# Kernel optimization log

Hardware: AMD Instinct MI355X
Metric: run time of the kernel (lower is better)

Reference implementation:

```python
import jax, jax.numpy as jnp
import numpy as np

# Hyperparameters matching init_kwargs
DIM = 1024
HEADS = 16
MEM_HIDDEN = 512
FF_DIM = 4096
CHUNK = 128
NPERSIST = 16
ALPHA = 0.02
THETA = 0.1
ETA = 0.9
B, T = 2, 1024


def _mem_read(x, p):
    """DeepMemory forward: 2-layer MLP dim->hidden->dim with SiLU between."""
    W1, b1, W2, b2 = p
    h = jax.nn.silu(x @ W1.T + b1)
    return h @ W2.T + b2


def setup_inputs() -> dict:
    key = jax.random.key(0)
    ks = jax.random.split(key, 16)
    s = 0.02  # weight init scale
    return {
        "x": jax.random.normal(ks[0], (B, T, DIM), jnp.float32),
        "Wqkv": jax.random.normal(ks[1], (3 * DIM, DIM), jnp.float32) * s,
        "mW1": jax.random.normal(ks[2], (MEM_HIDDEN, DIM), jnp.float32) * s,
        "mb1": jnp.zeros((MEM_HIDDEN,), jnp.float32),
        "mW2": jax.random.normal(ks[3], (DIM, MEM_HIDDEN), jnp.float32) * s,
        "mb2": jnp.zeros((DIM,), jnp.float32),
        "P": jax.random.normal(ks[4], (1, NPERSIST, DIM), jnp.float32),
        "Wqkv_attn": jax.random.normal(ks[5], (3 * DIM, DIM), jnp.float32) * s,
        "Wo": jax.random.normal(ks[6], (DIM, DIM), jnp.float32) * s,
        "ffW1": jax.random.normal(ks[7], (FF_DIM, DIM), jnp.float32) * s,
        "ffb1": jnp.zeros((FF_DIM,), jnp.float32),
        "ffW2": jax.random.normal(ks[8], (DIM, FF_DIM), jnp.float32) * s,
        "ffb2": jnp.zeros((DIM,), jnp.float32),
    }


def reference(x, Wqkv, mW1, mb1, mW2, mb2, P, Wqkv_attn, Wo, ffW1, ffb1, ffW2, ffb2):
    Bb, Tt, D = x.shape
    nC = Tt // CHUNK

    # shared qkv projection (bias-free Linear)
    qkv = x @ Wqkv.T                       # [B,T,3D]
    K = qkv[..., D:2 * D]
    V = qkv[..., 2 * D:]

    # chunked test-time memory writes: k,v are detached in the torch code
    Kc = jax.lax.stop_gradient(K).reshape(Bb, nC, CHUNK, D).transpose(1, 0, 2, 3)  # [nC,B,C,D]
    Vc = jax.lax.stop_gradient(V).reshape(Bb, nC, CHUNK, D).transpose(1, 0, 2, 3)

    params0 = tuple(jax.lax.stop_gradient(p) for p in (mW1, mb1, mW2, mb2))
    mom0 = tuple(jnp.zeros_like(p) for p in params0)

    def loss_fn(p, k, v):
        return jnp.mean((_mem_read(k, p) - v) ** 2)

    def step(carry, kv):
        p, m = carry
        k, v = kv
        g = jax.grad(loss_fn)(p, k, v)
        # momentum: s = eta*s - theta*g ; weight: w = (1-alpha)*w + s
        m = tuple(ETA * mi - THETA * gi for mi, gi in zip(m, g))
        p = tuple((1.0 - ALPHA) * pi + mi for pi, mi in zip(p, m))
        return (p, m), None

    (pf, _), _ = jax.lax.scan(step, (params0, mom0), (Kc, Vc))
    pf = jax.lax.stop_gradient(pf)  # fast weights are buffers (non-differentiable)

    # memory readout tokens for the whole segment
    Q = qkv[..., :D]
    mem_tok = _mem_read(Q, pf)             # [B,T,D]

    # concatenate persistent + memory + input tokens
    tokens = jnp.concatenate([jnp.broadcast_to(P, (Bb, NPERSIST, D)), mem_tok, x], axis=1)
    N = tokens.shape[1]                    # NPERSIST + 2T
    dh = D // HEADS

    # causal multi-head attention over the concatenated sequence
    aqkv = tokens @ Wqkv_attn.T            # [B,N,3D]
    q, k, v = jnp.split(aqkv, 3, axis=-1)
    to_heads = lambda t: t.reshape(Bb, N, HEADS, dh).transpose(0, 2, 1, 3)
    q, k, v = to_heads(q), to_heads(k), to_heads(v)
    scores = jnp.einsum('bhnd,bhmd->bhnm', q, k) / jnp.sqrt(jnp.float32(dh))
    causal = jnp.tril(jnp.ones((N, N), bool))
    scores = jnp.where(causal, scores, jnp.float32(-1e9))
    attn = jax.nn.softmax(scores, axis=-1)
    o = jnp.einsum('bhnm,bhmd->bhnd', attn, v).transpose(0, 2, 1, 3).reshape(Bb, N, D)
    y = o @ Wo.T

    # feed-forward (no residual in source)
    y = jax.nn.gelu(y @ ffW1.T + ffb1) @ ffW2.T + ffb2

    # drop persistent + memory tokens, gate by a fresh memory read
    out = y[:, NPERSIST + Tt:, :]          # [B,T,D]
    newQ = (out @ Wqkv.T)[..., :D]
    return out * _mem_read(newQ, pf)
```

## Files before the change

### kernel.cpp

```cpp
#include <hip/hip_runtime.h>
#include <math.h>

#define BATCH 2
#define TSEQ 1024
#define DIMD 1024
#define NPERS 16
#define NCH 8
#define NTOK 2064
#define ETA_C 0.9f
#define THETA_C 0.1f
#define ALPHA_C 0.02f

typedef __attribute__((ext_vector_type(4))) float f32x4;
typedef __attribute__((ext_vector_type(8))) short s16x8;
typedef unsigned short u16;

__device__ __forceinline__ u16 f2bf(float f) {
    unsigned int u = __float_as_uint(f);
    return (u16)((u + 0x7fffu + ((u >> 16) & 1u)) >> 16);
}
__device__ __forceinline__ float bf2f(u16 h) { return __uint_as_float(((unsigned)h) << 16); }
__device__ __forceinline__ void split2(float v, u16& h, u16& l) {
    h = f2bf(v); l = f2bf(v - bf2f(h));
}

static const size_t oRA = 0;
static const size_t oRB = 50724864;
static const size_t oRC = 67633152;
static const size_t oRD = 80216064;
static const size_t oRE = 96993280;
static const size_t oRF = 109576192;
static const size_t oRG = 113770496;
static const size_t oRH = 117970944;

static const size_t PW1 = 0, PB1 = 524288, PW2 = 524800, PB2 = 1049088, PSZ = 1050112;

__device__ __forceinline__ void gload_lds16(const u16* g, u16* l) {
    __builtin_amdgcn_global_load_lds(
        (const __attribute__((address_space(1))) unsigned int*)g,
        (__attribute__((address_space(3))) unsigned int*)l, 16, 0, 0);
}

__device__ __forceinline__ void xcd_swizzle(int& bx, int& by) {
    int gx = gridDim.x, nwg = gx * gridDim.y;
    int lid = blockIdx.y * gx + blockIdx.x;
    int t = lid;
    if ((nwg & 7) == 0) {
        int q = nwg >> 3;
        t = (lid & 7) * q + (lid >> 3);
    }
    bx = t % gx; by = t / gx;
}

__device__ __forceinline__ void stage_tile(const u16* sp, u16* buf, int rbase,
                                           int M, int clampM, int K, int k0,
                                           int wid, int lane) {
    const int lr = lane >> 2, lc = lane & 3;
    #pragma unroll
    for (int i = 0; i < 8; ++i) {
        int r = i * 16 + lr;
        int gr = rbase + r;
        if (clampM && gr >= M) gr = M - 1;
        int g = lc ^ ((r >> 1) & 3);
        gload_lds16(sp + (size_t)gr * K + k0 + g * 8, buf + wid * 4096 + i * 512);
    }
}

__device__ __forceinline__ void stage_tile64(const u16* sp, u16* buf, int rbase,
                                             int K, int k0, int wid, int lane) {
    const int lr = lane >> 3, lc = lane & 7;
    #pragma unroll
    for (int i = 0; i < 16; ++i) {
        int r = i * 8 + lr;
        int gr = rbase + r;
        int g = lc ^ (r & 7);
        gload_lds16(sp + (size_t)gr * K + k0 + g * 8, buf + wid * 8192 + i * 512);
    }
}

template<int NPROD>
__device__ __forceinline__ void mm_loop32(u16 lds[2][16384],
                const u16* sp, int rbase, int M, int clampM, int K,
                int kbeg, int kend, int wid, int lane, int wm, int wn,
                f32x4 acc[4][4]) {
    const int frow = lane & 15, kblk = lane >> 4;
    const int nt = (kend - kbeg) >> 5;
    const int doStage = (NPROD == 3) || (wid != 1);
    if (doStage) stage_tile(sp, lds[0], rbase, M, clampM, K, kbeg, wid, lane);
    for (int t = 0; t < nt; ++t) {
        __syncthreads();
        if (t + 1 < nt && doStage)
            stage_tile(sp, lds[(t + 1) & 1], rbase, M, clampM, K, kbeg + ((t + 1) << 5), wid, lane);
        const u16* cb = lds[t & 1];
        s16x8 bh[4], bl[4];
        #pragma unroll
        for (int ni = 0; ni < 4; ++ni) {
            int br = wn * 64 + ni * 16 + frow;
            int pc = kblk ^ ((br >> 1) & 3);
            bh[ni] = *(const s16x8*)&cb[2 * 4096 + br * 32 + pc * 8];
            bl[ni] = *(const s16x8*)&cb[3 * 4096 + br * 32 + pc * 8];
        }
        #pragma unroll
        for (int mi = 0; mi < 4; ++mi) {
            int ar = wm * 64 + mi * 16 + frow;
            int pc = kblk ^ ((ar >> 1) & 3);
            s16x8 ah = *(const s16x8*)&cb[0 * 4096 + ar * 32 + pc * 8];
            s16x8 al;
            if (NPROD == 3) al = *(const s16x8*)&cb[1 * 4096 + ar * 32 + pc * 8];
            #pragma unroll
            for (int ni = 0; ni < 4; ++ni) {
                acc[mi][ni] = __builtin_amdgcn_mfma_f32_16x16x32_bf16(ah, bh[ni], acc[mi][ni], 0, 0, 0);
                acc[mi][ni] = __builtin_amdgcn_mfma_f32_16x16x32_bf16(ah, bl[ni], acc[mi][ni], 0, 0, 0);
                if (NPROD == 3)
                    acc[mi][ni] = __builtin_amdgcn_mfma_f32_16x16x32_bf16(al, bh[ni], acc[mi][ni], 0, 0, 0);
            }
        }
    }
}

template<int ACTF, int WF32, int WSPLIT, int PARTIAL, int NPROD>
__global__ __launch_bounds__(256)
void gemm_mfma_k(const u16* __restrict__ Ah, const u16* __restrict__ Al,
                 const u16* __restrict__ Wh, const u16* __restrict__ Wl,
                 float* __restrict__ C, u16* __restrict__ Chi, u16* __restrict__ Clo,
                 int M, int N, int K, const float* __restrict__ bias)
{
    __shared__ u16 lds[2][16384];
    const int tid = threadIdx.x;
    const int lane = tid & 63, wid = tid >> 6;
    const int wm = wid >> 1, wn = wid & 1;
    int bx, by; xcd_swizzle(bx, by);
    const int row0 = by * 128, col0 = bx * 128;
    const u16* sp = (wid == 0) ? Ah : (wid == 1) ? Al : (wid == 2) ? Wh : Wl;
    const int rbase = (wid < 2) ? row0 : col0;
    const int clampM = (wid < 2) ? 1 : 0;
    f32x4 acc[4][4] = {};
    int kbeg = 0, kend = K;
    if (PARTIAL) {
        int Kseg = K / gridDim.z;
        kbeg = blockIdx.z * Kseg;
        kend = kbeg + Kseg;
    }
    mm_loop32<NPROD>(lds, sp, rbase, M, clampM, K, kbeg, kend, wid, lane, wm, wn, acc);

    const int erow = (lane >> 4) * 4, ecol = lane & 15;
    #pragma unroll
    for (int mi = 0; mi < 4; ++mi) {
        #pragma unroll
        for (int ni = 0; ni < 4; ++ni) {
            int c = col0 + wn * 64 + ni * 16 + ecol;
            float bv = (!PARTIAL && bias) ? bias[c] : 0.f;
            #pragma unroll
            for (int reg = 0; reg < 4; ++reg) {
                int r = row0 + wm * 64 + mi * 16 + erow + reg;
                if (r >= M) continue;
                float v = acc[mi][ni][reg] + bv;
                if (PARTIAL) {
                    C[((size_t)blockIdx.z * M + r) * N + c] = v;
                    continue;
                }
                if (ACTF == 1) v = v / (1.f + __expf(-v));
                else if (ACTF == 2) {
                    float u = 0.7978845608028654f * (v + 0.044715f * v * v * v);
                    v = 0.5f * v * (1.f + tanhf(u));
                }
                size_t o = (size_t)r * N + c;
                if (WF32) C[o] = v;
                if (WSPLIT) { u16 h, l; split2(v, h, l); Chi[o] = h; Clo[o] = l; }
            }
        }
    }
}

__global__ __launch_bounds__(256)
void gemm_qkv_k(const u16* __restrict__ Ah, const u16* __restrict__ Al,
                const u16* __restrict__ Wh, const u16* __restrict__ Wl,
                u16* __restrict__ Qh, u16* __restrict__ Ql,
                u16* __restrict__ kch, u16* __restrict__ kcl,
                u16* __restrict__ kcTh, u16* __restrict__ kcTl,
                float* __restrict__ Vb, int M, int N, int K)
{
    __shared__ u16 lds[2][16384];
    const int tid = threadIdx.x;
    const int lane = tid & 63, wid = tid >> 6;
    const int wm = wid >> 1, wn = wid & 1;
    int bx, by; xcd_swizzle(bx, by);
    const int row0 = by * 128, col0 = bx * 128;
    const u16* sp = (wid == 0) ? Ah : (wid == 1) ? Al : (wid == 2) ? Wh : Wl;
    const int rbase = (wid < 2) ? row0 : col0;
    f32x4 acc[4][4] = {};
    mm_loop32<3>(lds, sp, rbase, M, 0, K, 0, K, wid, lane, wm, wn, acc);

    const int erow = (lane >> 4) * 4, ecol = lane & 15;
    #pragma unroll
    for (int mi = 0; mi < 4; ++mi) {
        #pragma unroll
        for (int ni = 0; ni < 4; ++ni) {
            int c = col0 + wn * 64 + ni * 16 + ecol;
            #pragma unroll
            for (int reg = 0; reg < 4; ++reg) {
                int r = row0 + wm * 64 + mi * 16 + erow + reg;
                float v = acc[mi][ni][reg];
                int b = r >> 10, t = r & 1023;
                if (c < 1024) {
                    size_t o = (size_t)r * 1024 + c;
                    u16 h, l; split2(v, h, l); Qh[o] = h; Ql[o] = l;
                } else if (c < 2048) {
                    int d = c - 1024;
                    int ch = t >> 7, rr = t & 127;
                    size_t o = ((size_t)((ch * 2 + b) * 128 + rr)) * 1024 + d;
                    u16 h, l; split2(v, h, l);
                    kch[o] = h; kcl[o] = l;
                    size_t ot = (size_t)ch * 262144 + (size_t)d * 256 + b * 128 + rr;
                    kcTh[ot] = h; kcTl[ot] = l;
                } else {
                    int d = c - 2048;
                    int ch = t >> 7, rr = t & 127;
                    Vb[((size_t)((ch * 2 + b) * 128 + rr)) * 1024 + d] = v;
                }
            }
        }
    }
}

__global__ __launch_bounds__(256)
void gemm_aqkv_k(const u16* __restrict__ Ah, const u16* __restrict__ Al,
                 const u16* __restrict__ Wh, const u16* __restrict__ Wl,
                 u16* __restrict__ fQh, u16* __restrict__ fQl,
                 u16* __restrict__ fKh, u16* __restrict__ fKl,
                 u16* __restrict__ fVt, int M, int N, int K)
{
    __shared__ u16 lds[2][16384];
    const int tid = threadIdx.x;
    const int lane = tid & 63, wid = tid >> 6;
    const int wm = wid >> 1, wn = wid & 1;
    int bx, by; xcd_swizzle(bx, by);
    if (bx < 8 && ((by <= 7) || (by >= 17 && by <= 23))) return;
    const int row0 = by * 128, col0 = bx * 128;
    const u16* sp = (wid == 0) ? Ah : (wid == 1) ? Al : (wid == 2) ? Wh : Wl;
    const int rbase = (wid < 2) ? row0 : col0;
    const int clampM = (wid < 2) ? 1 : 0;
    f32x4 acc[4][4] = {};
    mm_loop32<2>(lds, sp, rbase, M, clampM, K, 0, K, wid, lane, wm, wn, acc);

    const int erow = (lane >> 4) * 4, ecol = lane & 15;
    #pragma unroll
    for (int mi = 0; mi < 4; ++mi) {
        #pragma unroll
        for (int ni = 0; ni < 4; ++ni) {
            int c = col0 + wn * 64 + ni * 16 + ecol;
            #pragma unroll
            for (int reg = 0; reg < 4; ++reg) {
                int r = row0 + wm * 64 + mi * 16 + erow + reg;
                if (r >= M) continue;
                float v = acc[mi][ni][reg];
                int b = (r >= 2064) ? 1 : 0;
                int n = r - b * 2064;
                if (c < 1024) {
                    if (n >= NPERS + TSEQ) {
                        int h = c >> 6, d = c & 63;
                        int row = n - (NPERS + TSEQ);
                        size_t o = (((size_t)(b * 16 + h)) * 1024 + row) * 64 + d;
                        u16 hh, ll; split2(0.125f * v, hh, ll);
                        fQh[o] = hh; fQl[o] = ll;
                    }
                } else if (c < 2048) {
                    int cc = c - 1024;
                    int h = cc >> 6, d = cc & 63;
                    size_t o = (((size_t)(b * 16 + h)) * NTOK + n) * 64 + d;
                    u16 hh, ll; split2(v, hh, ll);
                    fKh[o] = hh; fKl[o] = ll;
                } else {
                    int cc = c - 2048;
                    int h = cc >> 6, d = cc & 63;
                    fVt[(((size_t)(b * 16 + h)) * 64 + d) * NTOK + n] = f2bf(v);
                }
            }
        }
    }
}

template<int ACTF, int WF32, int WSPLIT>
__global__ __launch_bounds__(256)
void reduce_k(const float* __restrict__ Cp, int S,
              float* __restrict__ C, u16* __restrict__ Chi, u16* __restrict__ Clo,
              const float* __restrict__ bias, int M, int N)
{
    int i = blockIdx.x * 256 + threadIdx.x;
    int n4 = (int)((size_t)M * N / 4);
    if (i >= n4) return;
    size_t off = (size_t)i * 4;
    float4 v = *(const float4*)&Cp[off];
    for (int z = 1; z < S; ++z) {
        float4 u = *(const float4*)&Cp[(size_t)z * M * N + off];
        v.x += u.x; v.y += u.y; v.z += u.z; v.w += u.w;
    }
    int c = (int)(off % N);
    float vv[4] = {v.x, v.y, v.z, v.w};
    #pragma unroll
    for (int j = 0; j < 4; ++j) {
        float w = vv[j];
        if (bias) w += bias[c + j];
        if (ACTF == 1) w = w / (1.f + __expf(-w));
        else if (ACTF == 2) {
            float u = 0.7978845608028654f * (w + 0.044715f * w * w * w);
            w = 0.5f * w * (1.f + tanhf(u));
        }
        if (WF32) C[off + j] = w;
        if (WSPLIT) { u16 h, l; split2(w, h, l); Chi[off + j] = h; Clo[off + j] = l; }
    }
}

static void gemm_mfma(hipStream_t s, int act, int wf32, int wsplit,
                      const u16* Ah, const u16* Al, const u16* Wh, const u16* Wl,
                      float* C, u16* Ch, u16* Cl, int M, int N, int K,
                      const float* bias, int nprod = 3)
{
    dim3 g(N / 128, (M + 127) / 128), b(256);
    if (act == 0 && wf32 == 1 && wsplit == 0)
        gemm_mfma_k<0,1,0,0,3><<<g,b,0,s>>>(Ah,Al,Wh,Wl,C,Ch,Cl,M,N,K,bias);
    else if (act == 0 && wf32 == 1 && wsplit == 1)
        gemm_mfma_k<0,1,1,0,3><<<g,b,0,s>>>(Ah,Al,Wh,Wl,C,Ch,Cl,M,N,K,bias);
    else if (act == 0 && wf32 == 0 && wsplit == 1)
        gemm_mfma_k<0,0,1,0,3><<<g,b,0,s>>>(Ah,Al,Wh,Wl,C,Ch,Cl,M,N,K,bias);
    else if (act == 1)
        gemm_mfma_k<1,0,1,0,3><<<g,b,0,s>>>(Ah,Al,Wh,Wl,C,Ch,Cl,M,N,K,bias);
    else if (nprod == 2)
        gemm_mfma_k<2,0,1,0,2><<<g,b,0,s>>>(Ah,Al,Wh,Wl,C,Ch,Cl,M,N,K,bias);
    else
        gemm_mfma_k<2,0,1,0,3><<<g,b,0,s>>>(Ah,Al,Wh,Wl,C,Ch,Cl,M,N,K,bias);
}

static void gemm_mfma_sk(hipStream_t s, int act, int wf32, int wsplit,
                         const u16* Ah, const u16* Al, const u16* Wh, const u16* Wl,
                         float* C, u16* Ch, u16* Cl, int M, int N, int K,
                         const float* bias, int S, float* part, int nprod = 3)
{
    if (S <= 1) { gemm_mfma(s, act, wf32, wsplit, Ah, Al, Wh, Wl, C, Ch, Cl, M, N, K, bias, nprod); return; }
    dim3 g(N / 128, (M + 127) / 128, S), b(256);
    if (nprod == 2)
        gemm_mfma_k<0,0,0,1,2><<<g,b,0,s>>>(Ah,Al,Wh,Wl,part,nullptr,nullptr,M,N,K,nullptr);
    else
        gemm_mfma_k<0,0,0,1,3><<<g,b,0,s>>>(Ah,Al,Wh,Wl,part,nullptr,nullptr,M,N,K,nullptr);
    int n4 = (int)((size_t)M * N / 4);
    dim3 rg((n4 + 255) / 256), rb(256);
    if (act == 0 && wf32 == 1 && wsplit == 0)
        reduce_k<0,1,0><<<rg,rb,0,s>>>(part, S, C, Ch, Cl, bias, M, N);
    else if (act == 0 && wf32 == 1 && wsplit == 1)
        reduce_k<0,1,1><<<rg,rb,0,s>>>(part, S, C, Ch, Cl, bias, M, N);
    else if (act == 0 && wf32 == 0 && wsplit == 1)
        reduce_k<0,0,1><<<rg,rb,0,s>>>(part, S, C, Ch, Cl, bias, M, N);
    else if (act == 1)
        reduce_k<1,0,1><<<rg,rb,0,s>>>(part, S, C, Ch, Cl, bias, M, N);
    else
        reduce_k<2,0,1><<<rg,rb,0,s>>>(part, S, C, Ch, Cl, bias, M, N);
}

template<int MODE>
__device__ __forceinline__ void scan_body(u16* lds, int bx, int by,
                 const u16* __restrict__ Ah, const u16* __restrict__ Al,
                 const u16* __restrict__ Wh, const u16* __restrict__ Wl,
                 float* __restrict__ C, u16* __restrict__ Chi, u16* __restrict__ Clo,
                 u16* __restrict__ ChiT, u16* __restrict__ CloT,
                 const float* __restrict__ Zf, const float* __restrict__ add,
                 const float* __restrict__ bias, float* __restrict__ CP,
                 int M, int N, int K, float alpha)
{
    const int tid = threadIdx.x;
    const int lane = tid & 63, wid = tid >> 6;
    const int wm = wid >> 1, wn = wid & 1;
    const int row0 = by * 128, col0 = bx * 128;

    const u16* sp = (wid == 0) ? Ah : (wid == 1) ? Al : (wid == 2) ? Wh : Wl;
    const int rbase = (wid < 2) ? row0 : col0;

    f32x4 acc[4][4] = {};
    const int frow = lane & 15, kblk = lane >> 4;
    const int nt = K >> 6;

    stage_tile64(sp, lds, rbase, K, 0, wid, lane);

    for (int t = 0; t < nt; ++t) {
        __syncthreads();
        if (t + 1 < nt)
            stage_tile64(sp, lds + (((t + 1) & 1) << 15), rbase, K, (t + 1) << 6, wid, lane);
        const u16* cb = lds + ((t & 1) << 15);

        #pragma unroll
        for (int s = 0; s < 2; ++s) {
            s16x8 bh[4], bl[4];
            #pragma unroll
            for (int ni = 0; ni < 4; ++ni) {
                int br = wn * 64 + ni * 16 + frow;
                int pc = (s * 4 + kblk) ^ (br & 7);
                bh[ni] = *(const s16x8*)&cb[2 * 8192 + br * 64 + pc * 8];
                bl[ni] = *(const s16x8*)&cb[3 * 8192 + br * 64 + pc * 8];
            }
            #pragma unroll
            for (int mi = 0; mi < 4; ++mi) {
                int ar = wm * 64 + mi * 16 + frow;
                int pc = (s * 4 + kblk) ^ (ar & 7);
                s16x8 ah = *(const s16x8*)&cb[0 * 8192 + ar * 64 + pc * 8];
                s16x8 al = *(const s16x8*)&cb[1 * 8192 + ar * 64 + pc * 8];
                #pragma unroll
                for (int ni = 0; ni < 4; ++ni) {
                    acc[mi][ni] = __builtin_amdgcn_mfma_f32_16x16x32_bf16(ah, bh[ni], acc[mi][ni], 0, 0, 0);
                    acc[mi][ni] = __builtin_amdgcn_mfma_f32_16x16x32_bf16(ah, bl[ni], acc[mi][ni], 0, 0, 0);
                    acc[mi][ni] = __builtin_amdgcn_mfma_f32_16x16x32_bf16(al, bh[ni], acc[mi][ni], 0, 0, 0);
                }
            }
        }
    }

    const int erow = (lane >> 4) * 4, ecol = lane & 15;
    float csum[4] = {0.f, 0.f, 0.f, 0.f};
    #pragma unroll
    for (int mi = 0; mi < 4; ++mi) {
        #pragma unroll
        for (int ni = 0; ni < 4; ++ni) {
            int c = col0 + wn * 64 + ni * 16 + ecol;
            #pragma unroll
            for (int reg = 0; reg < 4; ++reg) {
                int r = row0 + wm * 64 + mi * 16 + erow + reg;
                float v = acc[mi][ni][reg];
                size_t o = (size_t)r * N + c;
                if (MODE == 1) {
                    v += bias[c];
                    C[o] = v;
                    float hv = v / (1.f + __expf(-v));
                    u16 h, l; split2(hv, h, l);
                    Chi[o] = h; Clo[o] = l;
                    size_t ot = (size_t)c * M + r;
                    ChiT[ot] = h; CloT[ot] = l;
                } else if (MODE == 2) {
                    v += bias[c] - add[o];
                    u16 h, l; split2(v, h, l);
                    Chi[o] = h; Clo[o] = l;
                    size_t ot = (size_t)c * M + r;
                    ChiT[ot] = h; CloT[ot] = l;
                    csum[ni] += v;
                } else if (MODE == 3) {
                    C[o] = alpha * v;
                } else {
                    v *= alpha;
                    float z = Zf[o];
                    float sg = 1.f / (1.f + __expf(-z));
                    v *= sg * (1.f + z * (1.f - sg));
                    u16 h, l; split2(v, h, l);
                    size_t ot = (size_t)c * M + r;
                    ChiT[ot] = h; CloT[ot] = l;
                    csum[ni] += v;
                }
            }
        }
    }
    if (MODE == 2 || MODE == 4) {
        #pragma unroll
        for (int ni = 0; ni < 4; ++ni) {
            float s = csum[ni];
            s += __shfl_xor(s, 16);
            s += __shfl_xor(s, 32);
            if ((lane >> 4) == 0) {
                int c = col0 + wn * 64 + ni * 16 + ecol;
                float w = (MODE == 2) ? alpha * s : s;
                CP[(size_t)(by * 2 + wm) * N + c] = w;
            }
        }
    }
}

template<int MODE>
__global__ __launch_bounds__(256)
void gemm_scan_k(const u16* __restrict__ Ah, const u16* __restrict__ Al,
                 const u16* __restrict__ Wh, const u16* __restrict__ Wl,
                 float* __restrict__ C, u16* __restrict__ Chi, u16* __restrict__ Clo,
                 u16* __restrict__ ChiT, u16* __restrict__ CloT,
                 const float* __restrict__ Zf, const float* __restrict__ add,
                 const float* __restrict__ bias, float* __restrict__ CP,
                 int M, int N, int K, float alpha)
{
    __shared__ u16 lds[2][32768];
    int bx, by; xcd_swizzle(bx, by);
    scan_body<MODE>(&lds[0][0], bx, by, Ah, Al, Wh, Wl, C, Chi, Clo, ChiT, CloT,
                    Zf, add, bias, CP, M, N, K, alpha);
}

__global__ __launch_bounds__(256)
void gemm_scan_pair_k(const u16* __restrict__ rTh, const u16* __restrict__ rTl,
                      const u16* __restrict__ hTh, const u16* __restrict__ hTl,
                      float* __restrict__ gW2,
                      const u16* __restrict__ rh_, const u16* __restrict__ rl_,
                      const u16* __restrict__ w2th, const u16* __restrict__ w2tl,
                      u16* __restrict__ dhTh, u16* __restrict__ dhTl,
                      const float* __restrict__ z1, float* __restrict__ cp1, float cs)
{
    __shared__ u16 lds[2][32768];
    if (blockIdx.y < 8) {
        scan_body<3>(&lds[0][0], blockIdx.x, blockIdx.y, rTh, rTl, hTh, hTl,
                     gW2, nullptr, nullptr, nullptr, nullptr, nullptr, nullptr,
                     nullptr, nullptr, 1024, 512, 256, cs);
    } else {
        scan_body<4>(&lds[0][0], blockIdx.x, blockIdx.y - 8, rh_, rl_, w2th, w2tl,
                     nullptr, nullptr, nullptr, dhTh, dhTl, z1, nullptr,
                     nullptr, cp1, 256, 512, 1024, cs);
    }
}

__global__ void cvt_split_k(const float* __restrict__ in, u16* __restrict__ hi,
                            u16* __restrict__ lo, int n4) {
    int i = blockIdx.x * 256 + threadIdx.x;
    if (i >= n4) return;
    float4 v = *(const float4*)&in[(size_t)i * 4];
    u16 h0,l0,h1,l1,h2,l2,h3,l3;
    split2(v.x,h0,l0); split2(v.y,h1,l1); split2(v.z,h2,l2); split2(v.w,h3,l3);
    ushort4 hv = {h0,h1,h2,h3}, lv = {l0,l1,l2,l3};
    *(ushort4*)&hi[(size_t)i * 4] = hv;
    *(ushort4*)&lo[(size_t)i * 4] = lv;
}
__global__ void transpose_split_k(const float* __restrict__ in, u16* __restrict__ outh,
                                  u16* __restrict__ outl, int R, int C) {
    __shared__ float t[32][33];
    const int c0 = blockIdx.x * 32, r0 = blockIdx.y * 32;
    const size_t zoff = (size_t)blockIdx.z * R * C;
    const int tx = threadIdx.x & 31, ty = threadIdx.x >> 5;
    #pragma unroll
    for (int p = 0; p < 4; ++p) {
        int r = ty + p * 8;
        t[r][tx] = in[zoff + (size_t)(r0 + r) * C + c0 + tx];
    }
    __syncthreads();
    #pragma unroll
    for (int p = 0; p < 4; ++p) {
        int cc = ty + p * 8;
        float v = t[tx][cc];
        u16 h, l; split2(v, h, l);
        size_t o = zoff + (size_t)(c0 + cc) * R + r0 + tx;
        outh[o] = h; outl[o] = l;
    }
}
__global__ void update3_k(float* __restrict__ p, float* __restrict__ mo,
                          const float* __restrict__ g,
                          const float* __restrict__ cp1, const float* __restrict__ cp2,
                          u16* __restrict__ w1h, u16* __restrict__ w1l,
                          u16* __restrict__ w2h, u16* __restrict__ w2l,
                          u16* __restrict__ w2th, u16* __restrict__ w2tl, int n) {
    int i = blockIdx.x * 256 + threadIdx.x;
    if (i >= n) return;
    float gi;
    if (i < 524288) gi = g[i];
    else if (i < 524800) {
        int j = i - 524288;
        gi = cp1[j] + cp1[512 + j] + cp1[1024 + j] + cp1[1536 + j];
    } else if (i < 1049088) gi = g[i];
    else {
        int j = i - 1049088;
        gi = cp2[j] + cp2[1024 + j] + cp2[2048 + j] + cp2[3072 + j];
    }
    float m = ETA_C * mo[i] - THETA_C * gi;
    mo[i] = m;
    float pv = (1.f - ALPHA_C) * p[i] + m;
    p[i] = pv;
    if (i < 524288) {
        u16 h, l; split2(pv, h, l); w1h[i] = h; w1l[i] = l;
    } else if (i >= 524800 && i < 1049088) {
        int j = i - 524800;
        u16 h, l; split2(pv, h, l);
        w2h[j] = h; w2l[j] = l;
        int tj = (j & 511) * 1024 + (j >> 9);
        w2th[tj] = h; w2tl[tj] = l;
    }
}
__global__ void tokens_split_k(const float* __restrict__ P, const float* __restrict__ memtok,
                               const float* __restrict__ x, u16* __restrict__ th,
                               u16* __restrict__ tl) {
    size_t idx = (size_t)blockIdx.x * 256 + threadIdx.x;
    int d = (int)(idx & 1023);
    int n = (int)((idx >> 10) % NTOK);
    int b = (int)(idx / ((size_t)NTOK * 1024));
    float v;
    if (n < NPERS)            v = P[(size_t)n * 1024 + d];
    else if (n < NPERS + TSEQ) v = memtok[((size_t)b * TSEQ + (n - NPERS)) * 1024 + d];
    else                      v = x[((size_t)b * TSEQ + (n - NPERS - TSEQ)) * 1024 + d];
    u16 h, l; split2(v, h, l); th[idx] = h; tl[idx] = l;
}
__global__ void mul_k(const float* __restrict__ a, const float* __restrict__ b,
                      float* __restrict__ o, int n) {
    int i = blockIdx.x * 256 + threadIdx.x;
    if (i < n) o[i] = a[i] * b[i];
}

__global__ __launch_bounds__(256)
void flash_part_k(const u16* __restrict__ Qsh, const u16* __restrict__ Qsl,
                  const u16* __restrict__ Ksh, const u16* __restrict__ Ksl,
                  const u16* __restrict__ Vts, float* __restrict__ Of,
                  float* __restrict__ Mf, float* __restrict__ Lf)
{
    __shared__ u16 lds[20480];
    u16* KH = lds;            u16* KL = lds + 4096;
    u16* VT = lds + 8192;
    u16* PH = lds + 12288;    u16* PL = lds + 16384;

    int lid = blockIdx.x + (blockIdx.y << 4) + (blockIdx.z << 8);
    int t1024 = ((lid & 7) << 7) | (lid >> 3);
    const int qt = t1024 & 15, h = (t1024 >> 4) & 15;
    const int zb = t1024 >> 8;
    const int b = zb >> 1, z = zb & 1;

    const int tid = threadIdx.x;
    const int lane = tid & 63, wid = tid >> 6;
    const int fr = lane & 15, kq = lane >> 4;
    const int bh = b * 16 + h;
    const int q0c = qt * 64;
    const int q0a = NPERS + TSEQ + q0c;
    const int ntile = ((q0a + 63) >> 6) + 1;
    const int half = ntile >> 1;
    const int jt0 = z ? half : 0;
    const int jt1 = z ? ntile : half;
    const int l8 = lane & 7, lr8 = lane >> 3;

    auto stageKV = [&](int jt) {
        const int j0 = jt * 64;
        #pragma unroll
        for (int jj = 0; jj < 6; ++jj) {
            int j = wid * 6 + jj;
            int buf = j >> 3, i8 = j & 7;
            if (buf < 2) {
                int row = i8 * 8 + lr8;
                int grow = j0 + row; if (grow > NTOK - 1) grow = NTOK - 1;
                int c = l8 ^ (row & 7);
                const u16* src = (buf == 0 ? Ksh : Ksl) +
                                 (((size_t)bh * NTOK + grow) << 6) + c * 8;
                gload_lds16(src, (buf == 0 ? KH : KL) + i8 * 512);
            } else {
                int d = i8 * 8 + lr8;
                int c = l8 ^ (d & 7);
                int col = j0 + c * 8; if (col > NTOK - 8) col = NTOK - 8;
                const u16* src = Vts + ((size_t)bh * 64 + d) * NTOK + col;
                gload_lds16(src, VT + i8 * 512);
            }
        }
    };

    s16x8 qh[2], ql[2];
    {
        const size_t qrow = ((size_t)bh * 1024 + q0c + wid * 16 + fr) << 6;
        #pragma unroll
        for (int kb = 0; kb < 2; ++kb) {
            qh[kb] = *(const s16x8*)&Qsh[qrow + (size_t)(kb * 4 + kq) * 8];
            ql[kb] = *(const s16x8*)&Qsl[qrow + (size_t)(kb * 4 + kq) * 8];
        }
    }

    f32x4 Oa[4] = {};
    float mrow[4], lrow[4];
    #pragma unroll
    for (int r = 0; r < 4; ++r) { mrow[r] = -INFINITY; lrow[r] = 0.f; }

    for (int jt = jt0; jt < jt1; ++jt) {
        const int j0 = jt * 64;
        stageKV(jt);
        __syncthreads();

        f32x4 sacc[4] = {};
        __builtin_amdgcn_s_setprio(1);
        #pragma unroll
        for (int nt = 0; nt < 4; ++nt) {
            #pragma unroll
            for (int kb = 0; kb < 2; ++kb) {
                int br = nt * 16 + fr;
                int sl = (kb * 4 + kq) ^ (fr & 7);
                s16x8 kh = *(const s16x8*)&KH[br * 64 + sl * 8];
                s16x8 kl = *(const s16x8*)&KL[br * 64 + sl * 8];
                sacc[nt] = __builtin_amdgcn_mfma_f32_16x16x32_bf16(qh[kb], kh, sacc[nt], 0, 0, 0);
                sacc[nt] = __builtin_amdgcn_mfma_f32_16x16x32_bf16(ql[kb], kh, sacc[nt], 0, 0, 0);
                sacc[nt] = __builtin_amdgcn_mfma_f32_16x16x32_bf16(qh[kb], kl, sacc[nt], 0, 0, 0);
            }
        }
        __builtin_amdgcn_s_setprio(0);

        #pragma unroll
        for (int r = 0; r < 4; ++r) {
            const int qloc = kq * 4 + r;
            const int qi = q0a + wid * 16 + qloc;
            float sv[4], tmax = -INFINITY;
            #pragma unroll
            for (int nt = 0; nt < 4; ++nt) {
                int kj = j0 + nt * 16 + fr;
                sv[nt] = (kj <= qi) ? sacc[nt][r] : -INFINITY;
                tmax = fmaxf(tmax, sv[nt]);
            }
            #pragma unroll
            for (int off = 1; off < 16; off <<= 1)
                tmax = fmaxf(tmax, __shfl_xor(tmax, off));
            float mnew = fmaxf(mrow[r], tmax);
            float scale = __expf(mrow[r] - mnew);
            float psum = 0.f;
            float p4[4];
            #pragma unroll
            for (int nt = 0; nt < 4; ++nt) { p4[nt] = __expf(sv[nt] - mnew); psum += p4[nt]; }
            #pragma unroll
            for (int off = 1; off < 16; off <<= 1)
                psum += __shfl_xor(psum, off);
            lrow[r] = lrow[r] * scale + psum;
            mrow[r] = mnew;
            #pragma unroll
            for (int dt = 0; dt < 4; ++dt) Oa[dt][r] *= scale;
            const int prow = wid * 16 + qloc;
            #pragma unroll
            for (int nt = 0; nt < 4; ++nt) {
                u16 ph, pl; split2(p4[nt], ph, pl);
                int col = nt * 16 + fr;
                int sl = (col >> 3) ^ (qloc & 7);
                int off = prow * 64 + sl * 8 + (col & 7);
                PH[off] = ph; PL[off] = pl;
            }
        }

        __builtin_amdgcn_s_setprio(1);
        #pragma unroll
        for (int kb = 0; kb < 2; ++kb) {
            int pr = wid * 16 + fr;
            int sl = (kb * 4 + kq) ^ (fr & 7);
            s16x8 pa = *(const s16x8*)&PH[pr * 64 + sl * 8];
            s16x8 pb = *(const s16x8*)&PL[pr * 64 + sl * 8];
            #pragma unroll
            for (int dt = 0; dt < 4; ++dt) {
                int vr = dt * 16 + fr;
                s16x8 vb = *(const s16x8*)&VT[vr * 64 + sl * 8];
                Oa[dt] = __builtin_amdgcn_mfma_f32_16x16x32_bf16(pa, vb, Oa[dt], 0, 0, 0);
                Oa[dt] = __builtin_amdgcn_mfma_f32_16x16x32_bf16(pb, vb, Oa[dt], 0, 0, 0);
            }
        }
        __builtin_amdgcn_s_setprio(0);
        __syncthreads();
    }

    const size_t obase = ((((size_t)z * 2 + b) * 16 + h) * 16 + qt) * 4096;
    const size_t mlb   = ((((size_t)z * 2 + b) * 16 + h) * 16 + qt) * 64;
    #pragma unroll
    for (int r = 0; r < 4; ++r) {
        int rl = wid * 16 + kq * 4 + r;
        if (fr == 0) { Mf[mlb + rl] = mrow[r]; Lf[mlb + rl] = lrow[r]; }
        #pragma unroll
        for (int dt = 0; dt < 4; ++dt)
            Of[obase + (size_t)rl * 64 + dt * 16 + fr] = Oa[dt][r];
    }
}

__global__ __launch_bounds__(256)
void flash_merge_k(const float* __restrict__ Of, const float* __restrict__ Mf,
                   const float* __restrict__ Lf, u16* __restrict__ oh, u16* __restrict__ ol)
{
    const int qt = blockIdx.x, h = blockIdx.y, b = blockIdx.z;
    const int tid = threadIdx.x;
    const int row = tid >> 2, quad = tid & 3;
    const size_t b0 = ((((size_t)0 * 2 + b) * 16 + h) * 16 + qt) * 4096 + (size_t)row * 64;
    const size_t b1 = ((((size_t)1 * 2 + b) * 16 + h) * 16 + qt) * 4096 + (size_t)row * 64;
    const size_t m0i = ((((size_t)0 * 2 + b) * 16 + h) * 16 + qt) * 64 + row;
    const size_t m1i = ((((size_t)1 * 2 + b) * 16 + h) * 16 + qt) * 64 + row;
    float m0 = Mf[m0i], m1 = Mf[m1i], l0 = Lf[m0i], l1 = Lf[m1i];
    float m = fmaxf(m0, m1);
    float e0 = __expf(m0 - m), e1 = __expf(m1 - m);
    float inv = 1.f / (l0 * e0 + l1 * e1);
    const size_t orow = ((size_t)(b * 1024 + qt * 64 + row)) * 1024 + h * 64;
    #pragma unroll
    for (int i = 0; i < 4; ++i) {
        int col = quad * 16 + i * 4;
        float4 v0 = *(const float4*)&Of[b0 + col];
        float4 v1 = *(const float4*)&Of[b1 + col];
        float o0 = (v0.x * e0 + v1.x * e1) * inv;
        float o1 = (v0.y * e0 + v1.y * e1) * inv;
        float o2 = (v0.z * e0 + v1.z * e1) * inv;
        float o3 = (v0.w * e0 + v1.w * e1) * inv;
        u16 h0,l0_,h1,l1_,h2,l2_,h3,l3_;
        split2(o0,h0,l0_); split2(o1,h1,l1_); split2(o2,h2,l2_); split2(o3,h3,l3_);
        ushort4 hv = {h0,h1,h2,h3}, lv = {l0_,l1_,l2_,l3_};
        *(ushort4*)&oh[orow + col] = hv;
        *(ushort4*)&ol[orow + col] = lv;
    }
}

extern "C" void kernel_launch(void* const* d_in, const int* in_sizes, int n_in,
                              void* d_out, int out_size, void* d_ws, size_t ws_size,
                              hipStream_t stream)
{
    const float* x     = (const float*)d_in[0];
    const float* Wqkv  = (const float*)d_in[1];
    const float* mW1   = (const float*)d_in[2];
    const float* mb1   = (const float*)d_in[3];
    const float* mW2   = (const float*)d_in[4];
    const float* mb2   = (const float*)d_in[5];
    const float* Pp    = (const float*)d_in[6];
    const float* Wqa   = (const float*)d_in[7];
    const float* Wo    = (const float*)d_in[8];
    const float* ffW1  = (const float*)d_in[9];
    const float* ffb1  = (const float*)d_in[10];
    const float* ffW2  = (const float*)d_in[11];
    const float* ffb2  = (const float*)d_in[12];
    char* wsb = (char*)d_ws;
    float* outp = (float*)d_out;

    float* z1    = (float*)(wsb + oRA);
    float* grd   = (float*)(wsb + oRA + 3145728);
    float* cp2   = (float*)(wsb + oRA + 7346176);
    float* cp1   = (float*)(wsb + oRA + 7362560);
    u16* hh_     = (u16*)(wsb + oRA + 8388608);
    u16* hl_     = (u16*)(wsb + oRA + 8650752);
    u16* hTh     = (u16*)(wsb + oRA + 9437184);
    u16* hTl     = (u16*)(wsb + oRA + 9699328);
    u16* rh_     = (u16*)(wsb + oRA + 10485760);
    u16* rl_     = (u16*)(wsb + oRA + 11010048);
    u16* rTh     = (u16*)(wsb + oRA + 11534336);
    u16* rTl     = (u16*)(wsb + oRA + 12058624);
    u16* dhTh    = (u16*)(wsb + oRA + 12582912);
    u16* dhTl    = (u16*)(wsb + oRA + 12845056);
    u16* kcTh    = (u16*)(wsb + oRA + 16777216);
    u16* kcTl    = (u16*)(wsb + oRA + 20971520);
    float* Of    = (float*)(wsb + oRA);
    float* Mf    = (float*)(wsb + oRA + 16777216);
    float* Lf    = (float*)(wsb + oRA + 17039360);
    u16* fVth    = (u16*)(wsb + oRA + 17825792);
    u16* fKl     = (u16*)(wsb + oRA + 26279936);
    u16* Woh     = (u16*)(wsb + oRA);
    u16* Wol     = (u16*)(wsb + oRA + 2097152);
    u16* ffhh    = (u16*)(wsb + oRA);
    u16* ffhl    = (u16*)(wsb + oRA + 16777216);
    u16* outbh   = (u16*)(wsb + oRA + 33554432);
    u16* outbl   = (u16*)(wsb + oRA + 37748736);
    u16* newQh   = (u16*)(wsb + oRA);
    u16* newQl   = (u16*)(wsb + oRA + 4194304);
    u16* hzh     = (u16*)(wsb + oRA + 8388608);
    u16* hzl     = (u16*)(wsb + oRA + 10485760);
    float* memq  = (float*)(wsb + oRA + 12582912);
    float* partA0 = (float*)(wsb + oRA);
    float* partA1 = (float*)(wsb + oRA + 4194304);
    float* partA2 = (float*)(wsb + oRA + 16777216);
    float* Vb    = (float*)(wsb + oRB + 8388608);
    u16* tokh    = (u16*)(wsb + oRB);
    u16* tokl    = (u16*)(wsb + oRB + 8454144);
    u16* oh      = (u16*)(wsb + oRB);
    u16* ol      = (u16*)(wsb + oRB + 4194304);
    u16* y1h     = (u16*)(wsb + oRB + 8388608);
    u16* y1l     = (u16*)(wsb + oRB + 12582912);
    float* partB = (float*)(wsb + oRB);
    u16* xh      = (u16*)(wsb + oRC);
    u16* xl      = (u16*)(wsb + oRC + 4194304);
    float* mom   = (float*)(wsb + oRC);
    u16* pW2Th   = (u16*)(wsb + oRC + 5242880);
    u16* pW2Tl   = (u16*)(wsb + oRC + 6291456);
    u16* Wqah    = (u16*)(wsb + oRC);
    u16* Wqal    = (u16*)(wsb + oRC + 6291456);
    u16* Qh      = (u16*)(wsb + oRD);
    u16* Ql      = (u16*)(wsb + oRD + 4194304);
    u16* kchh    = (u16*)(wsb + oRD + 8388608);
    u16* kchl    = (u16*)(wsb + oRD + 12582912);
    u16* t1h     = (u16*)(wsb + oRD + 8388608);
    u16* t1l     = (u16*)(wsb + oRD + 10485760);
    float* memtok= (float*)(wsb + oRD);
    u16* fKh     = (u16*)(wsb + oRD);
    u16* ffW1h   = (u16*)(wsb + oRD);
    u16* ffW1l   = (u16*)(wsb + oRD + 8388608);
    u16* ffW2h   = (u16*)(wsb + oRD);
    u16* ffW2l   = (u16*)(wsb + oRD + 8388608);
    u16* Wqkvh   = (u16*)(wsb + oRE);
    u16* Wqkvl   = (u16*)(wsb + oRE + 6291456);
    u16* pW1h    = (u16*)(wsb + oRF);
    u16* pW1l    = (u16*)(wsb + oRF + 1048576);
    u16* pW2h    = (u16*)(wsb + oRF + 2097152);
    u16* pW2l    = (u16*)(wsb + oRF + 3145728);
    float* par   = (float*)(wsb + oRG);
    float* outb  = (float*)(wsb + oRH);
    u16* fQh     = (u16*)(wsb + oRH);
    u16* fQl     = (u16*)(wsb + oRH + 4194304);

    hipMemcpyAsync(par + PW1, mW1, 524288 * sizeof(float), hipMemcpyDeviceToDevice, stream);
    hipMemcpyAsync(par + PB1, mb1, 512 * sizeof(float), hipMemcpyDeviceToDevice, stream);
    hipMemcpyAsync(par + PW2, mW2, 524288 * sizeof(float), hipMemcpyDeviceToDevice, stream);
    hipMemcpyAsync(par + PB2, mb2, 1024 * sizeof(float), hipMemcpyDeviceToDevice, stream);

    cvt_split_k<<<2048, 256, 0, stream>>>(x, xh, xl, 524288);
    cvt_split_k<<<3072, 256, 0, stream>>>(Wqkv, Wqkvh, Wqkvl, 786432);
    gemm_qkv_k<<<dim3(24, 16), 256, 0, stream>>>(xh, xl, Wqkvh, Wqkvl,
        Qh, Ql, kchh, kchl, kcTh, kcTl, Vb, 2048, 3072, 1024);

    hipMemsetAsync(mom, 0, PSZ * sizeof(float), stream);
    cvt_split_k<<<512, 256, 0, stream>>>(par + PW1, pW1h, pW1l, 131072);
    cvt_split_k<<<512, 256, 0, stream>>>(par + PW2, pW2h, pW2l, 131072);
    transpose_split_k<<<dim3(16, 32, 1), 256, 0, stream>>>(par + PW2, pW2Th, pW2Tl, 1024, 512);

    const float cs = 2.f / (float)(BATCH * 128 * DIMD);
    for (int c = 0; c < NCH; ++c) {
        const u16* kch = kchh + (size_t)c * 262144;
        const u16* kcl = kchl + (size_t)c * 262144;
        const u16* kth = kcTh + (size_t)c * 262144;
        const u16* ktl = kcTl + (size_t)c * 262144;
        const float* vc = Vb + (size_t)c * 262144;
        gemm_scan_k<1><<<dim3(4, 2), 256, 0, stream>>>(kch, kcl, pW1h, pW1l,
            z1, hh_, hl_, hTh, hTl, nullptr, nullptr, par + PB1, nullptr, 256, 512, 1024, 1.f);
        gemm_scan_k<2><<<dim3(8, 2), 256, 0, stream>>>(hh_, hl_, pW2h, pW2l,
            nullptr, rh_, rl_, rTh, rTl, nullptr, vc, par + PB2, cp2, 256, 1024, 512, cs);
        gemm_scan_pair_k<<<dim3(4, 10), 256, 0, stream>>>(rTh, rTl, hTh, hTl, grd + PW2,
            rh_, rl_, pW2Th, pW2Tl, dhTh, dhTl, z1, cp1, cs);
        gemm_scan_k<3><<<dim3(8, 4), 256, 0, stream>>>(dhTh, dhTl, kth, ktl,
            grd + PW1, nullptr, nullptr, nullptr, nullptr, nullptr, nullptr, nullptr, nullptr,
            512, 1024, 256, 1.f);
        update3_k<<<4102, 256, 0, stream>>>(par, mom, grd, cp1, cp2,
            pW1h, pW1l, pW2h, pW2l, pW2Th, pW2Tl, (int)PSZ);
    }

    gemm_mfma_sk(stream, 1, 0, 1, Qh, Ql, pW1h, pW1l, nullptr, t1h, t1l,
                 2048, 512, 1024, par + PB1, 4, partA2);
    gemm_mfma_sk(stream, 0, 1, 0, t1h, t1l, pW2h, pW2l, memtok, nullptr, nullptr,
                 2048, 1024, 512, par + PB2, 2, partA0);

    tokens_split_k<<<16512, 256, 0, stream>>>(Pp, memtok, x, tokh, tokl);
    cvt_split_k<<<3072, 256, 0, stream>>>(Wqa, Wqah, Wqal, 786432);
    gemm_aqkv_k<<<dim3(24, 33), 256, 0, stream>>>(tokh, tokl, Wqah, Wqal,
        fQh, fQl, fKh, fKl, fVth, 4128, 3072, 1024);

    flash_part_k<<<dim3(16, 16, 4), 256, 0, stream>>>(fQh, fQl, fKh, fKl, fVth, Of, Mf, Lf);
    flash_merge_k<<<dim3(16, 16, 2), 256, 0, stream>>>(Of, Mf, Lf, oh, ol);

    cvt_split_k<<<1024, 256, 0, stream>>>(Wo, Woh, Wol, 262144);
    gemm_mfma_sk(stream, 0, 0, 1, oh, ol, Woh, Wol, nullptr, y1h, y1l,
                 2048, 1024, 1024, nullptr, 2, partA1);
    cvt_split_k<<<4096, 256, 0, stream>>>(ffW1, ffW1h, ffW1l, 1048576);
    gemm_mfma(stream, 2, 0, 1, y1h, y1l, ffW1h, ffW1l, nullptr, ffhh, ffhl,
              2048, 4096, 1024, ffb1, 2);
    cvt_split_k<<<4096, 256, 0, stream>>>(ffW2, ffW2h, ffW2l, 1048576);
    gemm_mfma_sk(stream, 0, 1, 1, ffhh, ffhl, ffW2h, ffW2l, outb, outbh, outbl,
                 2048, 1024, 4096, ffb2, 2, partB, 2);

    gemm_mfma_sk(stream, 0, 0, 1, outbh, outbl, Wqkvh, Wqkvl, nullptr, newQh, newQl,
                 2048, 1024, 1024, nullptr, 2, partB);
    gemm_mfma_sk(stream, 1, 0, 1, newQh, newQl, pW1h, pW1l, nullptr, hzh, hzl,
                 2048, 512, 1024, par + PB1, 4, partB);
    gemm_mfma_sk(stream, 0, 1, 0, hzh, hzl, pW2h, pW2l, memq, nullptr, nullptr,
                 2048, 1024, 512, par + PB2, 2, partB);
    mul_k<<<8192, 256, 0, stream>>>(outb, memq, outp, 2097152);
}
```

Before: 1.361 ms.

## Double-buffer flash K/V staging and fuse memory-token split into reduction

The flash attention partial kernel now uses two LDS buffers for K/V and prefetches the next tile while computing on the current one, dropping one barrier per iteration. Separately, the split-K reduction of the memory-read GEMM now writes bf16 hi/lo pairs directly into the token buffer, so the fp32 memtok intermediate is gone and the token split kernel only handles the persistent and input rows. This is meant to hide global-to-LDS latency and cut an extra memory round trip, at the cost of more LDS per block (64KB), which may lower occupancy.

Result: no change. 1.358 ms (-0.2%).

```diff
diff --git a/kernel.cpp b/kernel.cpp
--- a/kernel.cpp
+++ b/kernel.cpp
@@ -309,6 +309,27 @@
         if (WF32) C[off + j] = w;
         if (WSPLIT) { u16 h, l; split2(w, h, l); Chi[off + j] = h; Clo[off + j] = l; }
     }
+}
+
+__global__ __launch_bounds__(256)
+void reduce_tok_k(const float* __restrict__ Cp, const float* __restrict__ bias,
+                  u16* __restrict__ th, u16* __restrict__ tl)
+{
+    int i = blockIdx.x * 256 + threadIdx.x;
+    if (i >= 524288) return;
+    size_t off = (size_t)i * 4;
+    float4 v = *(const float4*)&Cp[off];
+    float4 u = *(const float4*)&Cp[2097152 + off];
+    v.x += u.x; v.y += u.y; v.z += u.z; v.w += u.w;
+    int r = (int)(off >> 10), c = (int)(off & 1023);
+    int b = r >> 10, t = r & 1023;
+    size_t orow = (((size_t)(b * NTOK + NPERS + t)) << 10) + c;
+    float vv[4] = {v.x + bias[c], v.y + bias[c + 1], v.z + bias[c + 2], v.w + bias[c + 3]};
+    u16 h0,l0,h1,l1,h2,l2,h3,l3;
+    split2(vv[0],h0,l0); split2(vv[1],h1,l1); split2(vv[2],h2,l2); split2(vv[3],h3,l3);
+    ushort4 hv = {h0,h1,h2,h3}, lv = {l0,l1,l2,l3};
+    *(ushort4*)&th[orow] = hv;
+    *(ushort4*)&tl[orow] = lv;
 }
 
 static void gemm_mfma(hipStream_t s, int act, int wf32, int wsplit,
@@ -570,18 +591,18 @@
         w2th[tj] = h; w2tl[tj] = l;
     }
 }
-__global__ void tokens_split_k(const float* __restrict__ P, const float* __restrict__ memtok,
-                               const float* __restrict__ x, u16* __restrict__ th,
-                               u16* __restrict__ tl) {
+__global__ void tokens_px_k(const float* __restrict__ P, const float* __restrict__ x,
+                            u16* __restrict__ th, u16* __restrict__ tl) {
     size_t idx = (size_t)blockIdx.x * 256 + threadIdx.x;
+    if (idx >= (size_t)2 * 1040 * 1024) return;
     int d = (int)(idx & 1023);
-    int n = (int)((idx >> 10) % NTOK);
-    int b = (int)(idx / ((size_t)NTOK * 1024));
-    float v;
-    if (n < NPERS)            v = P[(size_t)n * 1024 + d];
-    else if (n < NPERS + TSEQ) v = memtok[((size_t)b * TSEQ + (n - NPERS)) * 1024 + d];
-    else                      v = x[((size_t)b * TSEQ + (n - NPERS - TSEQ)) * 1024 + d];
-    u16 h, l; split2(v, h, l); th[idx] = h; tl[idx] = l;
+    int rl = (int)((idx >> 10) % 1040);
+    int b = (int)(idx / ((size_t)1040 * 1024));
+    float v; int n;
+    if (rl < NPERS) { v = P[(size_t)rl * 1024 + d]; n = rl; }
+    else { int t = rl - NPERS; v = x[((size_t)b * TSEQ + t) * 1024 + d]; n = NPERS + TSEQ + t; }
+    size_t o = (((size_t)(b * NTOK + n)) << 10) + d;
+    u16 h, l; split2(v, h, l); th[o] = h; tl[o] = l;
 }
 __global__ void mul_k(const float* __restrict__ a, const float* __restrict__ b,
                       float* __restrict__ o, int n) {
@@ -595,10 +616,9 @@
                   const u16* __restrict__ Vts, float* __restrict__ Of,
                   float* __restrict__ Mf, float* __restrict__ Lf)
 {
-    __shared__ u16 lds[20480];
-    u16* KH = lds;            u16* KL = lds + 4096;
-    u16* VT = lds + 8192;
-    u16* PH = lds + 12288;    u16* PL = lds + 16384;
+    __shared__ u16 lds[32768];
+    u16* KV0 = lds;           u16* KV1 = lds + 12288;
+    u16* PH = lds + 24576;    u16* PL = lds + 28672;
 
     int lid = blockIdx.x + (blockIdx.y << 4) + (blockIdx.z << 8);
     int t1024 = ((lid & 7) << 7) | (lid >> 3);
@@ -618,7 +638,7 @@
     const int jt1 = z ? ntile : half;
     const int l8 = lane & 7, lr8 = lane >> 3;
 
-    auto stageKV = [&](int jt) {
+    auto stageKV = [&](int jt, u16* kvb) {
         const int j0 = jt * 64;
         #pragma unroll
         for (int jj = 0; jj < 6; ++jj) {
@@ -630,13 +650,13 @@
                 int c = l8 ^ (row & 7);
                 const u16* src = (buf == 0 ? Ksh : Ksl) +
                                  (((size_t)bh * NTOK + grow) << 6) + c * 8;
-                gload_lds16(src, (buf == 0 ? KH : KL) + i8 * 512);
+                gload_lds16(src, kvb + buf * 4096 + i8 * 512);
             } else {
                 int d = i8 * 8 + lr8;
                 int c = l8 ^ (d & 7);
                 int col = j0 + c * 8; if (col > NTOK - 8) col = NTOK - 8;
                 const u16* src = Vts + ((size_t)bh * 64 + d) * NTOK + col;
-                gload_lds16(src, VT + i8 * 512);
+                gload_lds16(src, kvb + 8192 + i8 * 512);
             }
         }
     };
@@ -656,10 +676,16 @@
     #pragma unroll
     for (int r = 0; r < 4; ++r) { mrow[r] = -INFINITY; lrow[r] = 0.f; }
 
+    stageKV(jt0, KV0);
+    __syncthreads();
+
     for (int jt = jt0; jt < jt1; ++jt) {
         const int j0 = jt * 64;
-        stageKV(jt);
-        __syncthreads();
+        const int idx = jt - jt0;
+        if (idx) __syncthreads();
+        if (jt + 1 < jt1) stageKV(jt + 1, (idx & 1) ? KV0 : KV1);
+        u16* kvb = (idx & 1) ? KV1 : KV0;
+        u16* KH = kvb; u16* KL = kvb + 4096; u16* VT = kvb + 8192;
 
         f32x4 sacc[4] = {};
         __builtin_amdgcn_s_setprio(1);
@@ -732,7 +758,6 @@
             }
         }
         __builtin_amdgcn_s_setprio(0);
-        __syncthreads();
     }
 
     const size_t obase = ((((size_t)z * 2 + b) * 16 + h) * 16 + qt) * 4096;
@@ -856,7 +881,6 @@
     u16* kchl    = (u16*)(wsb + oRD + 12582912);
     u16* t1h     = (u16*)(wsb + oRD + 8388608);
     u16* t1l     = (u16*)(wsb + oRD + 10485760);
-    float* memtok= (float*)(wsb + oRD);
     u16* fKh     = (u16*)(wsb + oRD);
     u16* ffW1h   = (u16*)(wsb + oRD);
     u16* ffW1l   = (u16*)(wsb + oRD + 8388608);
@@ -910,10 +934,14 @@
 
     gemm_mfma_sk(stream, 1, 0, 1, Qh, Ql, pW1h, pW1l, nullptr, t1h, t1l,
                  2048, 512, 1024, par + PB1, 4, partA2);
-    gemm_mfma_sk(stream, 0, 1, 0, t1h, t1l, pW2h, pW2l, memtok, nullptr, nullptr,
-                 2048, 1024, 512, par + PB2, 2, partA0);
-
-    tokens_split_k<<<16512, 256, 0, stream>>>(Pp, memtok, x, tokh, tokl);
+    {
+        dim3 g(8, 16, 2), b(256);
+        gemm_mfma_k<0,0,0,1,3><<<g, b, 0, stream>>>(t1h, t1l, pW2h, pW2l,
+            partA0, nullptr, nullptr, 2048, 1024, 512, nullptr);
+        reduce_tok_k<<<2048, 256, 0, stream>>>(partA0, par + PB2, tokh, tokl);
+    }
+
+    tokens_px_k<<<8320, 256, 0, stream>>>(Pp, x, tokh, tokl);
     cvt_split_k<<<3072, 256, 0, stream>>>(Wqa, Wqah, Wqal, 786432);
     gemm_aqkv_k<<<dim3(24, 33), 256, 0, stream>>>(tokh, tokl, Wqah, Wqal,
         fQh, fQl, fKh, fKl, fVth, 4128, 3072, 1024);
```
